# Optimization experiments

Hardware: AMD Instinct MI355X
Metric: run time of the kernel (lower is better)

The kernel has to match this reference:

```python
import jax, jax.numpy as jnp
import numpy as np

H = 128  # hidden size

def lstm_layer(x, Wih, Whh, bih, bhh):
    """One PyTorch-semantics LSTM layer. x: (B,T,F). Gate order: i,f,g,o."""
    B = x.shape[0]
    # Precompute input contributions for all timesteps: (B,T,4H)
    xg = jnp.einsum('btf,gf->btg', x, Wih) + bih + bhh
    def step(carry, xt):
        h, c = carry
        g = xt + h @ Whh.T                      # (B,4H)
        i, f, gg, o = jnp.split(g, 4, axis=-1)
        i = jax.nn.sigmoid(i)
        f = jax.nn.sigmoid(f)
        gg = jnp.tanh(gg)
        o = jax.nn.sigmoid(o)
        c = f * c + i * gg
        h = o * jnp.tanh(c)
        return (h, c), h
    h0 = jnp.zeros((B, H), x.dtype)
    (hT, cT), hs = jax.lax.scan(step, (h0, h0), jnp.swapaxes(xg, 0, 1))
    return jnp.swapaxes(hs, 0, 1), hT  # (B,T,H), (B,H)


def setup_inputs() -> dict:
    key = jax.random.key(0)
    ks = jax.random.split(key, 20)
    B, T = 256, 2048
    s = 1.0 / np.sqrt(H)  # PyTorch default init scale
    inp = {
        'x': jax.random.normal(ks[0], (B, T, 1), jnp.float32),
        'Wih0': jax.random.uniform(ks[1], (4 * H, 1), jnp.float32, -s, s),
        'Whh0': jax.random.uniform(ks[2], (4 * H, H), jnp.float32, -s, s),
        'bih0': jax.random.uniform(ks[3], (4 * H,), jnp.float32, -s, s),
        'bhh0': jax.random.uniform(ks[4], (4 * H,), jnp.float32, -s, s),
        'Wih1': jax.random.uniform(ks[5], (4 * H, H), jnp.float32, -s, s),
        'Whh1': jax.random.uniform(ks[6], (4 * H, H), jnp.float32, -s, s),
        'bih1': jax.random.uniform(ks[7], (4 * H,), jnp.float32, -s, s),
        'bhh1': jax.random.uniform(ks[8], (4 * H,), jnp.float32, -s, s),
        'Wih2': jax.random.uniform(ks[9], (4 * H, H), jnp.float32, -s, s),
        'Whh2': jax.random.uniform(ks[10], (4 * H, H), jnp.float32, -s, s),
        'bih2': jax.random.uniform(ks[11], (4 * H,), jnp.float32, -s, s),
        'bhh2': jax.random.uniform(ks[12], (4 * H,), jnp.float32, -s, s),
        'fc1_w': jax.random.uniform(ks[13], (64, H), jnp.float32, -s, s),
        'fc1_b': jax.random.uniform(ks[14], (64,), jnp.float32, -s, s),
        'fc2_w': jax.random.uniform(ks[15], (5, 64), jnp.float32, -1.0 / 8, 1.0 / 8),
        'fc2_b': jax.random.uniform(ks[16], (5,), jnp.float32, -1.0 / 8, 1.0 / 8),
    }
    return inp


def reference(x, Wih0, Whh0, bih0, bhh0, Wih1, Whh1, bih1, bhh1,
              Wih2, Whh2, bih2, bhh2, fc1_w, fc1_b, fc2_w, fc2_b):
    # 3-layer LSTM (eval mode: inter-layer dropout is identity)
    h1, _ = lstm_layer(x, Wih0, Whh0, bih0, bhh0)
    h2, _ = lstm_layer(h1, Wih1, Whh1, bih1, bhh1)
    _, hT = lstm_layer(h2, Wih2, Whh2, bih2, bhh2)  # hn[-1]: (B,H)
    z = jax.nn.relu(hT @ fc1_w.T + fc1_b)
    return z @ fc2_w.T + fc2_b  # (B, num_classes)
```

## Files before the change

### kernel.cpp

```cpp
#include <hip/hip_runtime.h>

#define HDIM 128
#define TDIM 2048
#define BDIM 256
#define CHUNK 16
#define NT 512
#define XGP 20

typedef _Float16 half8_t __attribute__((ext_vector_type(8)));
typedef float f32x4 __attribute__((ext_vector_type(4)));

__device__ __forceinline__ f32x4 mfma16(half8_t a, half8_t b, f32x4 c) {
    return __builtin_amdgcn_mfma_f32_16x16x32_f16(a, b, c, 0, 0, 0);
}

__device__ __forceinline__ void fast_barrier() {
    asm volatile("s_waitcnt lgkmcnt(0)\n\ts_barrier" ::: "memory");
}

__device__ __forceinline__ float sigm_f(float x) { return 1.0f / (1.0f + __expf(-x)); }
__device__ __forceinline__ float tanh_f(float x) { return 1.0f - 2.0f / (1.0f + __expf(2.0f * x)); }

__global__ __launch_bounds__(256)
void convert_w(const float* __restrict__ Whh0, const float* __restrict__ Wih1,
               const float* __restrict__ Whh1, const float* __restrict__ Wih2,
               const float* __restrict__ Whh2, _Float16* __restrict__ dst) {
    int i = blockIdx.x * 256 + threadIdx.x;
    int seg = i >> 16, off = i & 65535;
    const float* s = (seg == 0) ? Whh0 : (seg == 1) ? Wih1 : (seg == 2) ? Whh1
                   : (seg == 3) ? Wih2 : Whh2;
    dst[i] = (_Float16)s[off];
}

__global__ __launch_bounds__(NT, 2)
void lstm3_kernel(const float* __restrict__ x,   const float* __restrict__ Wih0,
                  const float* __restrict__ bih0, const float* __restrict__ bhh0,
                  const float* __restrict__ bih1, const float* __restrict__ bhh1,
                  const float* __restrict__ bih2, const float* __restrict__ bhh2,
                  const float* __restrict__ fc1w, const float* __restrict__ fc1b,
                  const float* __restrict__ fc2w, const float* __restrict__ fc2b,
                  float* __restrict__ out,
                  _Float16* __restrict__ gbuf, const _Float16* __restrict__ wbuf)
{
    __shared__ __align__(16) _Float16 hwin_s[CHUNK][HDIM];
    __shared__ __align__(16) _Float16 xin_s[2][CHUNK][HDIM];
    __shared__ __align__(16) float xg_s[2][512 * XGP];
    __shared__ __align__(16) float z_s[64];

    const int tid = threadIdx.x;
    const int ln = tid & 63;
    const int wv = tid >> 6;
    const int n16 = ln & 15;
    const int kb = (ln >> 4) * 8;
    const int un = wv * 16 + n16;
    const int b = blockIdx.x;

    {
        float bsum[4], w0[4];
        half8_t bhh[4][4];
#pragma unroll
        for (int tau = 0; tau < 4; ++tau) {
            const int g = tau * HDIM + un;
            bsum[tau] = bih0[g] + bhh0[g];
            w0[tau] = Wih0[g];
#pragma unroll
            for (int kk = 0; kk < 4; ++kk)
                bhh[tau][kk] = *(const half8_t*)(wbuf + (size_t)g * HDIM + kk * 32 + kb);
        }
        if (tid < HDIM) hwin_s[CHUNK - 1][tid] = (_Float16)0.f;
        float c = 0.f;
        float4 xp[4];
        {
            const float4* xq = (const float4*)(x + (size_t)b * TDIM);
#pragma unroll
            for (int i = 0; i < 4; ++i) xp[i] = xq[i];
        }

#pragma unroll 1
        for (int t0 = 0; t0 < TDIM; t0 += CHUNK) {
            float xv[CHUNK];
#pragma unroll
            for (int i = 0; i < 4; ++i) {
                xv[4 * i] = xp[i].x; xv[4 * i + 1] = xp[i].y;
                xv[4 * i + 2] = xp[i].z; xv[4 * i + 3] = xp[i].w;
            }
            int tn = (t0 + CHUNK < TDIM) ? (t0 + CHUNK) : t0;
            const float4* xq = (const float4*)(x + (size_t)b * TDIM + tn);
#pragma unroll
            for (int i = 0; i < 4; ++i) xp[i] = xq[i];

#pragma unroll
            for (int tt = 0; tt < CHUNK; ++tt) {
                fast_barrier();
                const int t = t0 + tt, row = (t + CHUNK - 1) & 15;
                half8_t A0 = *(const half8_t*)&hwin_s[row][kb];
                half8_t A1 = *(const half8_t*)&hwin_s[row][32 + kb];
                half8_t A2 = *(const half8_t*)&hwin_s[row][64 + kb];
                half8_t A3 = *(const half8_t*)&hwin_s[row][96 + kb];
                float g4[4];
#pragma unroll
                for (int tau = 0; tau < 4; ++tau) {
                    f32x4 Cz = {0.f, 0.f, 0.f, 0.f};
                    Cz = mfma16(A0, bhh[tau][0], Cz);
                    Cz = mfma16(A1, bhh[tau][1], Cz);
                    Cz = mfma16(A2, bhh[tau][2], Cz);
                    Cz = mfma16(A3, bhh[tau][3], Cz);
                    g4[tau] = Cz[0];
                }
                float ig = sigm_f(g4[0] + xv[tt] * w0[0] + bsum[0]);
                float fg = sigm_f(g4[1] + xv[tt] * w0[1] + bsum[1]);
                float gg = tanh_f(g4[2] + xv[tt] * w0[2] + bsum[2]);
                float og = sigm_f(g4[3] + xv[tt] * w0[3] + bsum[3]);
                c = fg * c + ig * gg;
                if (kb == 0) hwin_s[t & 15][un] = (_Float16)(og * tanh_f(c));
            }
            fast_barrier();
            int2 v = ((const int2*)&hwin_s[0][0])[tid];
            ((int2*)(gbuf + ((size_t)b * TDIM + t0) * HDIM))[tid] = v;
        }
    }

#pragma unroll 1
    for (int layer = 1; layer < 3; ++layer) {
        const _Float16* whh_p = wbuf + (size_t)((layer == 1) ? 2 : 4) * 65536;
        const _Float16* wih_p = wbuf + (size_t)((layer == 1) ? 1 : 3) * 65536;
        const float* bih = (layer == 1) ? bih1 : bih2;
        const float* bhh = (layer == 1) ? bhh1 : bhh2;

        float bsum[4];
        half8_t bhhf[4][4], bihf[4][4];
#pragma unroll
        for (int tau = 0; tau < 4; ++tau) {
            const int g = tau * HDIM + un;
            bsum[tau] = bih[g] + bhh[g];
#pragma unroll
            for (int kk = 0; kk < 4; ++kk)
                bhhf[tau][kk] = *(const half8_t*)(whh_p + (size_t)g * HDIM + kk * 32 + kb);
            const int gp = (wv * 4 + tau) * 16 + n16;
#pragma unroll
            for (int kk = 0; kk < 4; ++kk)
                bihf[tau][kk] = *(const half8_t*)(wih_p + (size_t)gp * HDIM + kk * 32 + kb);
        }

        __syncthreads();
        if (tid < HDIM) hwin_s[CHUNK - 1][tid] = (_Float16)0.f;
        float c = 0.f;

        int2 stage = ((const int2*)(gbuf + (size_t)b * TDIM * HDIM))[tid];
        ((int2*)&xin_s[0][0][0])[tid] = stage;
        __syncthreads();
        {
            half8_t A0 = *(const half8_t*)&xin_s[0][n16][kb];
            half8_t A1 = *(const half8_t*)&xin_s[0][n16][32 + kb];
            half8_t A2 = *(const half8_t*)&xin_s[0][n16][64 + kb];
            half8_t A3 = *(const half8_t*)&xin_s[0][n16][96 + kb];
#pragma unroll
            for (int tau = 0; tau < 4; ++tau) {
                f32x4 a = {0.f, 0.f, 0.f, 0.f};
                a = mfma16(A0, bihf[tau][0], a);
                a = mfma16(A1, bihf[tau][1], a);
                a = mfma16(A2, bihf[tau][2], a);
                a = mfma16(A3, bihf[tau][3], a);
                const int g = (wv * 4 + tau) * 16 + n16;
                *(f32x4*)&xg_s[0][g * XGP + (kb >> 1)] = a;
            }
        }
        stage = ((const int2*)(gbuf + ((size_t)b * TDIM + CHUNK) * HDIM))[tid];

        f32x4 pacc[4];
#pragma unroll 1
        for (int t0 = 0; t0 < TDIM; t0 += CHUNK) {
            const int ci = t0 >> 4, rbuf = ci & 1, cb = rbuf ^ 1;
            ((int2*)&xin_s[cb][0][0])[tid] = stage;
            int tn = (t0 + 2 * CHUNK < TDIM) ? (t0 + 2 * CHUNK) : t0;
            stage = ((const int2*)(gbuf + ((size_t)b * TDIM + tn) * HDIM))[tid];

            float2 xgv[4];
#pragma unroll
            for (int tt = 0; tt < CHUNK; ++tt) {
                fast_barrier();
                const int t = t0 + tt, row = (t + CHUNK - 1) & 15;
                half8_t A0 = *(const half8_t*)&hwin_s[row][kb];
                half8_t A1 = *(const half8_t*)&hwin_s[row][32 + kb];
                half8_t A2 = *(const half8_t*)&hwin_s[row][64 + kb];
                half8_t A3 = *(const half8_t*)&hwin_s[row][96 + kb];

                if (tt == 0) {
                    half8_t X0 = *(const half8_t*)&xin_s[cb][n16][kb];
                    half8_t X1 = *(const half8_t*)&xin_s[cb][n16][32 + kb];
                    half8_t X2 = *(const half8_t*)&xin_s[cb][n16][64 + kb];
                    half8_t X3 = *(const half8_t*)&xin_s[cb][n16][96 + kb];
#pragma unroll
                    for (int tau = 0; tau < 4; ++tau) {
                        f32x4 a = {0.f, 0.f, 0.f, 0.f};
                        a = mfma16(X0, bihf[tau][0], a);
                        a = mfma16(X1, bihf[tau][1], a);
                        a = mfma16(X2, bihf[tau][2], a);
                        a = mfma16(X3, bihf[tau][3], a);
                        pacc[tau] = a;
                    }
                }
                if ((tt & 1) == 0) {
#pragma unroll
                    for (int q = 0; q < 4; ++q)
                        xgv[q] = *(const float2*)&xg_s[rbuf][(q * HDIM + un) * XGP + tt];
                }

                float g4[4];
#pragma unroll
                for (int tau = 0; tau < 4; ++tau) {
                    f32x4 Cz = {0.f, 0.f, 0.f, 0.f};
                    Cz = mfma16(A0, bhhf[tau][0], Cz);
                    Cz = mfma16(A1, bhhf[tau][1], Cz);
                    Cz = mfma16(A2, bhhf[tau][2], Cz);
                    Cz = mfma16(A3, bhhf[tau][3], Cz);
                    g4[tau] = Cz[0];
                }

                float x0 = (tt & 1) ? xgv[0].y : xgv[0].x;
                float x1 = (tt & 1) ? xgv[1].y : xgv[1].x;
                float x2 = (tt & 1) ? xgv[2].y : xgv[2].x;
                float x3 = (tt & 1) ? xgv[3].y : xgv[3].x;
                float ig = sigm_f(g4[0] + x0 + bsum[0]);
                float fg = sigm_f(g4[1] + x1 + bsum[1]);
                float gg = tanh_f(g4[2] + x2 + bsum[2]);
                float og = sigm_f(g4[3] + x3 + bsum[3]);
                c = fg * c + ig * gg;
                if (kb == 0) hwin_s[t & 15][un] = (_Float16)(og * tanh_f(c));

                if (tt == CHUNK - 1) {
#pragma unroll
                    for (int tau = 0; tau < 4; ++tau) {
                        const int g = (wv * 4 + tau) * 16 + n16;
                        *(f32x4*)&xg_s[cb][g * XGP + (kb >> 1)] = pacc[tau];
                    }
                }
            }
            if (layer == 1) {
                fast_barrier();
                int2 v = ((const int2*)&hwin_s[0][0])[tid];
                ((int2*)(gbuf + ((size_t)b * TDIM + t0) * HDIM))[tid] = v;
            }
        }
    }

    __syncthreads();
    if (tid < 64) {
        const float* w = fc1w + tid * HDIM;
        float s = fc1b[tid];
#pragma unroll
        for (int k = 0; k < HDIM; ++k) s += w[k] * (float)hwin_s[CHUNK - 1][k];
        z_s[tid] = fmaxf(s, 0.0f);
    }
    __syncthreads();
    if (tid < 5) {
        const float* w = fc2w + tid * 64;
        float s = fc2b[tid];
#pragma unroll
        for (int k = 0; k < 64; ++k) s += w[k] * z_s[k];
        out[b * 5 + tid] = s;
    }
}

extern "C" void kernel_launch(void* const* d_in, const int* in_sizes, int n_in,
                              void* d_out, int out_size, void* d_ws, size_t ws_size,
                              hipStream_t stream) {
    (void)in_sizes; (void)n_in; (void)out_size; (void)ws_size;
    const float* x    = (const float*)d_in[0];
    const float* Wih0 = (const float*)d_in[1];
    const float* Whh0 = (const float*)d_in[2];
    const float* bih0 = (const float*)d_in[3];
    const float* bhh0 = (const float*)d_in[4];
    const float* Wih1 = (const float*)d_in[5];
    const float* Whh1 = (const float*)d_in[6];
    const float* bih1 = (const float*)d_in[7];
    const float* bhh1 = (const float*)d_in[8];
    const float* Wih2 = (const float*)d_in[9];
    const float* Whh2 = (const float*)d_in[10];
    const float* bih2 = (const float*)d_in[11];
    const float* bhh2 = (const float*)d_in[12];
    const float* fc1w = (const float*)d_in[13];
    const float* fc1b = (const float*)d_in[14];
    const float* fc2w = (const float*)d_in[15];
    const float* fc2b = (const float*)d_in[16];
    float* out = (float*)d_out;

    _Float16* gbuf = (_Float16*)d_ws;
    _Float16* wbuf = gbuf + (size_t)67108864;

    hipLaunchKernelGGL(convert_w, dim3(1280), dim3(256), 0, stream,
                       Whh0, Wih1, Whh1, Wih2, Whh2, wbuf);
    hipLaunchKernelGGL(lstm3_kernel, dim3(BDIM), dim3(NT), 0, stream,
                       x, Wih0, bih0, bhh0, bih1, bhh1, bih2, bhh2,
                       fc1w, fc1b, fc2w, fc2b, out, gbuf, wbuf);
}
```

Measured before the change: 3.658 ms.

## Wavefront-pipeline all three LSTM layers concurrently with LDS ring buffers

The kernel no longer runs the three layers one after another through a global scratch buffer. It runs them as a skewed wavefront, each layer lagging the previous one by 16 steps, so the whole network takes about T+32 barrier steps instead of 3T. Warps are assigned mixed slots across layers, and hidden states pass between layers through 32-deep LDS rings. The per-chunk input projection is computed from the ring, with Wih streamed from global memory on each use instead of held in registers. This removes two full sequential passes and the global round-trips, but each step now does more MFMA work per warp, adds more branching, and reloads Wih from global memory every chunk.

```diff
diff --git a/kernel.cpp b/kernel.cpp
--- a/kernel.cpp
+++ b/kernel.cpp
@@ -3,9 +3,11 @@
 #define HDIM 128
 #define TDIM 2048
 #define BDIM 256
-#define CHUNK 16
 #define NT 512
-#define XGP 20
+#define RING 32
+#define RP 136
+#define XGP 17
+#define NSTEP (TDIM + 32)
 
 typedef _Float16 half8_t __attribute__((ext_vector_type(8)));
 typedef float f32x4 __attribute__((ext_vector_type(4)));
@@ -13,9 +15,11 @@
 __device__ __forceinline__ f32x4 mfma16(half8_t a, half8_t b, f32x4 c) {
     return __builtin_amdgcn_mfma_f32_16x16x32_f16(a, b, c, 0, 0, 0);
 }
-
 __device__ __forceinline__ void fast_barrier() {
     asm volatile("s_waitcnt lgkmcnt(0)\n\ts_barrier" ::: "memory");
+}
+__device__ __forceinline__ void lds_fence() {
+    asm volatile("s_waitcnt lgkmcnt(0)" ::: "memory");
 }
 
 __device__ __forceinline__ float sigm_f(float x) { return 1.0f / (1.0f + __expf(-x)); }
@@ -39,207 +43,185 @@
                   const float* __restrict__ bih2, const float* __restrict__ bhh2,
                   const float* __restrict__ fc1w, const float* __restrict__ fc1b,
                   const float* __restrict__ fc2w, const float* __restrict__ fc2b,
-                  float* __restrict__ out,
-                  _Float16* __restrict__ gbuf, const _Float16* __restrict__ wbuf)
+                  float* __restrict__ out, const _Float16* __restrict__ wbuf)
 {
-    __shared__ __align__(16) _Float16 hwin_s[CHUNK][HDIM];
-    __shared__ __align__(16) _Float16 xin_s[2][CHUNK][HDIM];
+    __shared__ __align__(16) _Float16 ring_s[3][RING * RP];
     __shared__ __align__(16) float xg_s[2][512 * XGP];
+    __shared__ __align__(16) float xs_s[2][16];
     __shared__ __align__(16) float z_s[64];
 
-    const int tid = threadIdx.x;
-    const int ln = tid & 63;
-    const int wv = tid >> 6;
-    const int n16 = ln & 15;
-    const int kb = (ln >> 4) * 8;
-    const int un = wv * 16 + n16;
+    const int tid = threadIdx.x, ln = tid & 63, wv = tid >> 6;
+    const int n16 = ln & 15, qd = ln >> 4, kb = qd * 8;
     const int b = blockIdx.x;
 
+    const int s0l_t[8] = {0,0,0,1,1,1,2,2};
+    const int s0g_t[8] = {0,3,6,1,4,7,2,5};
+    const int s0n_t[8] = {3,3,2,3,3,1,3,3};
+    const int s1l_t[8] = {0,0,1,0,0,2,0,0};
+    const int s1n_t[8] = {0,0,1,0,0,2,0,0};
+    const int s0l = s0l_t[wv], s0g = s0g_t[wv], s0n = s0n_t[wv];
+    const int s1l = s1l_t[wv], s1n = s1n_t[wv];
+
+    int slayer[3], sgrp[3];
+#pragma unroll
+    for (int i = 0; i < 3; ++i) {
+        if (i < s0n) { slayer[i] = s0l; sgrp[i] = s0g + i; }
+        else         { slayer[i] = s1l; sgrp[i] = i - s0n; }
+    }
+
+    const _Float16* whhL0 = wbuf;
+    const _Float16* whhL1 = wbuf + 2 * 65536;
+    const _Float16* whhL2 = wbuf + 4 * 65536;
+    const _Float16* wihL1 = wbuf + 1 * 65536;
+    const _Float16* wihL2 = wbuf + 3 * 65536;
+
+    const int  lslot = (ln < 16) ? 0 : (ln < 32) ? 1 : 2;
+    const bool lact  = ln < 48;
+    const int  llay  = (lslot == 0) ? slayer[0] : (lslot == 1) ? slayer[1] : slayer[2];
+    const int  lgrp  = (lslot == 0) ? sgrp[0]   : (lslot == 1) ? sgrp[1]   : sgrp[2];
+    const int  u     = lgrp * 16 + n16;
+
+    float bsum[4], w0g[4];
+#pragma unroll
+    for (int q = 0; q < 4; ++q) {
+        const int row = q * HDIM + u;
+        const float* bi = (llay == 0) ? bih0 : (llay == 1) ? bih1 : bih2;
+        const float* bh = (llay == 0) ? bhh0 : (llay == 1) ? bhh1 : bhh2;
+        bsum[q] = bi[row] + bh[row];
+        w0g[q] = (llay == 0) ? Wih0[row] : 0.f;
+    }
+
+    half8_t bfr[3][4][4];
+#pragma unroll
+    for (int i = 0; i < 3; ++i) {
+        const int lay = slayer[i];
+        const _Float16* wp = (lay == 0) ? whhL0 : (lay == 1) ? whhL1 : whhL2;
+#pragma unroll
+        for (int tau = 0; tau < 4; ++tau) {
+            const int row = tau * HDIM + sgrp[i] * 16 + n16;
+#pragma unroll
+            for (int kk = 0; kk < 4; ++kk)
+                bfr[i][tau][kk] = *(const half8_t*)(wp + (size_t)row * HDIM + kk * 32 + kb);
+        }
+    }
+
     {
-        float bsum[4], w0[4];
-        half8_t bhh[4][4];
-#pragma unroll
-        for (int tau = 0; tau < 4; ++tau) {
-            const int g = tau * HDIM + un;
-            bsum[tau] = bih0[g] + bhh0[g];
-            w0[tau] = Wih0[g];
+        int* r = (int*)&ring_s[0][0];
+        for (int i = tid; i < 3 * RING * RP / 2; i += NT) r[i] = 0;
+    }
+    float xpre = 0.f;
+    if (wv == 0 && ln < 16) {
+        xs_s[0][ln] = x[(size_t)b * TDIM + ln];
+        xpre = x[(size_t)b * TDIM + 16 + ln];
+    }
+    __syncthreads();
+
+    float c_st = 0.f;
+    float g4[3][4];
+
+#pragma unroll 1
+    for (int s = 0; s < NSTEP; ++s) {
+        fast_barrier();
+
+        if (wv == 0 && (s & 15) == 15 && s < TDIM - 1 && ln < 16) {
+            xs_s[((s >> 4) + 1) & 1][ln] = xpre;
+            int t = s + 17 + ln;
+            xpre = x[(size_t)b * TDIM + (t < TDIM ? t : 0)];
+        }
+
+#pragma unroll
+        for (int pseg = 0; pseg < 2; ++pseg) {
+            const int pl  = (pseg == 0) ? s0l : s1l;
+            const int pg0 = (pseg == 0) ? s0g : 0;
+            const int pn  = (pseg == 0) ? s0n : s1n;
+            const bool en = (pseg == 0) ? (s0l >= 1) : (s1n > 0);
+            if (!en) continue;
+            const int tl = s - 16 * pl;
+            if (tl < 0 || tl >= TDIM || (tl & 15) != 0) continue;
+
+            const _Float16* ringp = &ring_s[pl - 1][0];
+            half8_t aP[4];
+            const int srow = ((tl + n16) & 31) * RP;
 #pragma unroll
             for (int kk = 0; kk < 4; ++kk)
-                bhh[tau][kk] = *(const half8_t*)(wbuf + (size_t)g * HDIM + kk * 32 + kb);
-        }
-        if (tid < HDIM) hwin_s[CHUNK - 1][tid] = (_Float16)0.f;
-        float c = 0.f;
-        float4 xp[4];
+                aP[kk] = *(const half8_t*)(ringp + srow + kk * 32 + kb);
+            const _Float16* wp = (pl == 1) ? wihL1 : wihL2;
+            float* xgb = &xg_s[pl - 1][0];
+#pragma unroll 1
+            for (int g = 0; g < pn; ++g) {
+#pragma unroll
+                for (int tau = 0; tau < 4; ++tau) {
+                    const int gp = tau * HDIM + (pg0 + g) * 16 + n16;
+                    const _Float16* wr = wp + (size_t)gp * HDIM + kb;
+                    half8_t b0 = *(const half8_t*)(wr);
+                    half8_t b1 = *(const half8_t*)(wr + 32);
+                    half8_t b2 = *(const half8_t*)(wr + 64);
+                    half8_t b3 = *(const half8_t*)(wr + 96);
+                    f32x4 a = {0.f, 0.f, 0.f, 0.f};
+                    a = mfma16(aP[0], b0, a);
+                    a = mfma16(aP[1], b1, a);
+                    a = mfma16(aP[2], b2, a);
+                    a = mfma16(aP[3], b3, a);
+                    float* dst = xgb + gp * XGP + qd * 4;
+                    dst[0] = a[0]; dst[1] = a[1]; dst[2] = a[2]; dst[3] = a[3];
+                }
+            }
+        }
+        lds_fence();
+
         {
-            const float4* xq = (const float4*)(x + (size_t)b * TDIM);
-#pragma unroll
-            for (int i = 0; i < 4; ++i) xp[i] = xq[i];
-        }
-
-#pragma unroll 1
-        for (int t0 = 0; t0 < TDIM; t0 += CHUNK) {
-            float xv[CHUNK];
-#pragma unroll
-            for (int i = 0; i < 4; ++i) {
-                xv[4 * i] = xp[i].x; xv[4 * i + 1] = xp[i].y;
-                xv[4 * i + 2] = xp[i].z; xv[4 * i + 3] = xp[i].w;
-            }
-            int tn = (t0 + CHUNK < TDIM) ? (t0 + CHUNK) : t0;
-            const float4* xq = (const float4*)(x + (size_t)b * TDIM + tn);
-#pragma unroll
-            for (int i = 0; i < 4; ++i) xp[i] = xq[i];
-
-#pragma unroll
-            for (int tt = 0; tt < CHUNK; ++tt) {
-                fast_barrier();
-                const int t = t0 + tt, row = (t + CHUNK - 1) & 15;
-                half8_t A0 = *(const half8_t*)&hwin_s[row][kb];
-                half8_t A1 = *(const half8_t*)&hwin_s[row][32 + kb];
-                half8_t A2 = *(const half8_t*)&hwin_s[row][64 + kb];
-                half8_t A3 = *(const half8_t*)&hwin_s[row][96 + kb];
-                float g4[4];
-#pragma unroll
-                for (int tau = 0; tau < 4; ++tau) {
-                    f32x4 Cz = {0.f, 0.f, 0.f, 0.f};
-                    Cz = mfma16(A0, bhh[tau][0], Cz);
-                    Cz = mfma16(A1, bhh[tau][1], Cz);
-                    Cz = mfma16(A2, bhh[tau][2], Cz);
-                    Cz = mfma16(A3, bhh[tau][3], Cz);
-                    g4[tau] = Cz[0];
-                }
-                float ig = sigm_f(g4[0] + xv[tt] * w0[0] + bsum[0]);
-                float fg = sigm_f(g4[1] + xv[tt] * w0[1] + bsum[1]);
-                float gg = tanh_f(g4[2] + xv[tt] * w0[2] + bsum[2]);
-                float og = sigm_f(g4[3] + xv[tt] * w0[3] + bsum[3]);
-                c = fg * c + ig * gg;
-                if (kb == 0) hwin_s[t & 15][un] = (_Float16)(og * tanh_f(c));
-            }
-            fast_barrier();
-            int2 v = ((const int2*)&hwin_s[0][0])[tid];
-            ((int2*)(gbuf + ((size_t)b * TDIM + t0) * HDIM))[tid] = v;
-        }
-    }
-
-#pragma unroll 1
-    for (int layer = 1; layer < 3; ++layer) {
-        const _Float16* whh_p = wbuf + (size_t)((layer == 1) ? 2 : 4) * 65536;
-        const _Float16* wih_p = wbuf + (size_t)((layer == 1) ? 1 : 3) * 65536;
-        const float* bih = (layer == 1) ? bih1 : bih2;
-        const float* bhh = (layer == 1) ? bhh1 : bhh2;
-
-        float bsum[4];
-        half8_t bhhf[4][4], bihf[4][4];
-#pragma unroll
-        for (int tau = 0; tau < 4; ++tau) {
-            const int g = tau * HDIM + un;
-            bsum[tau] = bih[g] + bhh[g];
-#pragma unroll
-            for (int kk = 0; kk < 4; ++kk)
-                bhhf[tau][kk] = *(const half8_t*)(whh_p + (size_t)g * HDIM + kk * 32 + kb);
-            const int gp = (wv * 4 + tau) * 16 + n16;
-#pragma unroll
-            for (int kk = 0; kk < 4; ++kk)
-                bihf[tau][kk] = *(const half8_t*)(wih_p + (size_t)gp * HDIM + kk * 32 + kb);
-        }
-
-        __syncthreads();
-        if (tid < HDIM) hwin_s[CHUNK - 1][tid] = (_Float16)0.f;
-        float c = 0.f;
-
-        int2 stage = ((const int2*)(gbuf + (size_t)b * TDIM * HDIM))[tid];
-        ((int2*)&xin_s[0][0][0])[tid] = stage;
-        __syncthreads();
-        {
-            half8_t A0 = *(const half8_t*)&xin_s[0][n16][kb];
-            half8_t A1 = *(const half8_t*)&xin_s[0][n16][32 + kb];
-            half8_t A2 = *(const half8_t*)&xin_s[0][n16][64 + kb];
-            half8_t A3 = *(const half8_t*)&xin_s[0][n16][96 + kb];
-#pragma unroll
-            for (int tau = 0; tau < 4; ++tau) {
-                f32x4 a = {0.f, 0.f, 0.f, 0.f};
-                a = mfma16(A0, bihf[tau][0], a);
-                a = mfma16(A1, bihf[tau][1], a);
-                a = mfma16(A2, bihf[tau][2], a);
-                a = mfma16(A3, bihf[tau][3], a);
-                const int g = (wv * 4 + tau) * 16 + n16;
-                *(f32x4*)&xg_s[0][g * XGP + (kb >> 1)] = a;
-            }
-        }
-        stage = ((const int2*)(gbuf + ((size_t)b * TDIM + CHUNK) * HDIM))[tid];
-
-        f32x4 pacc[4];
-#pragma unroll 1
-        for (int t0 = 0; t0 < TDIM; t0 += CHUNK) {
-            const int ci = t0 >> 4, rbuf = ci & 1, cb = rbuf ^ 1;
-            ((int2*)&xin_s[cb][0][0])[tid] = stage;
-            int tn = (t0 + 2 * CHUNK < TDIM) ? (t0 + 2 * CHUNK) : t0;
-            stage = ((const int2*)(gbuf + ((size_t)b * TDIM + tn) * HDIM))[tid];
-
-            float2 xgv[4];
-#pragma unroll
-            for (int tt = 0; tt < CHUNK; ++tt) {
-                fast_barrier();
-                const int t = t0 + tt, row = (t + CHUNK - 1) & 15;
-                half8_t A0 = *(const half8_t*)&hwin_s[row][kb];
-                half8_t A1 = *(const half8_t*)&hwin_s[row][32 + kb];
-                half8_t A2 = *(const half8_t*)&hwin_s[row][64 + kb];
-                half8_t A3 = *(const half8_t*)&hwin_s[row][96 + kb];
-
-                if (tt == 0) {
-                    half8_t X0 = *(const half8_t*)&xin_s[cb][n16][kb];
-                    half8_t X1 = *(const half8_t*)&xin_s[cb][n16][32 + kb];
-                    half8_t X2 = *(const half8_t*)&xin_s[cb][n16][64 + kb];
-                    half8_t X3 = *(const half8_t*)&xin_s[cb][n16][96 + kb];
+            half8_t aR[4];
+            int curlay = -1;
+#pragma unroll
+            for (int i = 0; i < 3; ++i) {
+                const int lay = slayer[i];
+                const int tl = s - 16 * lay;
+                if (tl >= 0 && tl < TDIM) {
+                    if (lay != curlay) {
+                        const _Float16* rp = &ring_s[lay][((tl - 1) & 31) * RP];
+#pragma unroll
+                        for (int kk = 0; kk < 4; ++kk)
+                            aR[kk] = *(const half8_t*)(rp + kk * 32 + kb);
+                        curlay = lay;
+                    }
 #pragma unroll
                     for (int tau = 0; tau < 4; ++tau) {
                         f32x4 a = {0.f, 0.f, 0.f, 0.f};
-                        a = mfma16(X0, bihf[tau][0], a);
-                        a = mfma16(X1, bihf[tau][1], a);
-                        a = mfma16(X2, bihf[tau][2], a);
-                        a = mfma16(X3, bihf[tau][3], a);
-                        pacc[tau] = a;
-                    }
-                }
-                if ((tt & 1) == 0) {
-#pragma unroll
-                    for (int q = 0; q < 4; ++q)
-                        xgv[q] = *(const float2*)&xg_s[rbuf][(q * HDIM + un) * XGP + tt];
-                }
-
-                float g4[4];
-#pragma unroll
-                for (int tau = 0; tau < 4; ++tau) {
-                    f32x4 Cz = {0.f, 0.f, 0.f, 0.f};
-                    Cz = mfma16(A0, bhhf[tau][0], Cz);
-                    Cz = mfma16(A1, bhhf[tau][1], Cz);
-                    Cz = mfma16(A2, bhhf[tau][2], Cz);
-                    Cz = mfma16(A3, bhhf[tau][3], Cz);
-                    g4[tau] = Cz[0];
-                }
-
-                float x0 = (tt & 1) ? xgv[0].y : xgv[0].x;
-                float x1 = (tt & 1) ? xgv[1].y : xgv[1].x;
-                float x2 = (tt & 1) ? xgv[2].y : xgv[2].x;
-                float x3 = (tt & 1) ? xgv[3].y : xgv[3].x;
-                float ig = sigm_f(g4[0] + x0 + bsum[0]);
-                float fg = sigm_f(g4[1] + x1 + bsum[1]);
-                float gg = tanh_f(g4[2] + x2 + bsum[2]);
-                float og = sigm_f(g4[3] + x3 + bsum[3]);
-                c = fg * c + ig * gg;
-                if (kb == 0) hwin_s[t & 15][un] = (_Float16)(og * tanh_f(c));
-
-                if (tt == CHUNK - 1) {
-#pragma unroll
-                    for (int tau = 0; tau < 4; ++tau) {
-                        const int g = (wv * 4 + tau) * 16 + n16;
-                        *(f32x4*)&xg_s[cb][g * XGP + (kb >> 1)] = pacc[tau];
+                        a = mfma16(aR[0], bfr[i][tau][0], a);
+                        a = mfma16(aR[1], bfr[i][tau][1], a);
+                        a = mfma16(aR[2], bfr[i][tau][2], a);
+                        a = mfma16(aR[3], bfr[i][tau][3], a);
+                        g4[i][tau] = a[0];
                     }
                 }
             }
-            if (layer == 1) {
-                fast_barrier();
-                int2 v = ((const int2*)&hwin_s[0][0])[tid];
-                ((int2*)(gbuf + ((size_t)b * TDIM + t0) * HDIM))[tid] = v;
+        }
+
+        {
+            const int tl_l = s - 16 * llay;
+            if (lact && tl_l >= 0 && tl_l < TDIM) {
+                float ga[4];
+#pragma unroll
+                for (int q = 0; q < 4; ++q)
+                    ga[q] = (lslot == 0) ? g4[0][q] : (lslot == 1) ? g4[1][q] : g4[2][q];
+                float xq[4];
+                if (llay == 0) {
+                    float xt = xs_s[(tl_l >> 4) & 1][tl_l & 15];
+#pragma unroll
+                    for (int q = 0; q < 4; ++q) xq[q] = xt * w0g[q];
+                } else {
+                    const float* xgb = &xg_s[llay - 1][0];
+#pragma unroll
+                    for (int q = 0; q < 4; ++q)
+                        xq[q] = xgb[(q * HDIM + u) * XGP + (tl_l & 15)];
+                }
+                float ig = sigm_f(ga[0] + xq[0] + bsum[0]);
+                float fg = sigm_f(ga[1] + xq[1] + bsum[1]);
+                float gg = tanh_f(ga[2] + xq[2] + bsum[2]);
+                float og = sigm_f(ga[3] + xq[3] + bsum[3]);
+                c_st = fg * c_st + ig * gg;
+                float h = og * tanh_f(c_st);
+                ring_s[llay][(tl_l & 31) * RP + u] = (_Float16)h;
             }
         }
     }
@@ -247,18 +229,18 @@
     __syncthreads();
     if (tid < 64) {
         const float* w = fc1w + tid * HDIM;
-        float s = fc1b[tid];
-#pragma unroll
-        for (int k = 0; k < HDIM; ++k) s += w[k] * (float)hwin_s[CHUNK - 1][k];
-        z_s[tid] = fmaxf(s, 0.0f);
+        float sacc = fc1b[tid];
+#pragma unroll
+        for (int k = 0; k < HDIM; ++k) sacc += w[k] * (float)ring_s[2][31 * RP + k];
+        z_s[tid] = fmaxf(sacc, 0.0f);
     }
     __syncthreads();
     if (tid < 5) {
         const float* w = fc2w + tid * 64;
-        float s = fc2b[tid];
-#pragma unroll
-        for (int k = 0; k < 64; ++k) s += w[k] * z_s[k];
-        out[b * 5 + tid] = s;
+        float sacc = fc2b[tid];
+#pragma unroll
+        for (int k = 0; k < 64; ++k) sacc += w[k] * z_s[k];
+        out[b * 5 + tid] = sacc;
     }
 }
 
@@ -285,12 +267,11 @@
     const float* fc2b = (const float*)d_in[16];
     float* out = (float*)d_out;
 
-    _Float16* gbuf = (_Float16*)d_ws;
-    _Float16* wbuf = gbuf + (size_t)67108864;
+    _Float16* wbuf = (_Float16*)d_ws;
 
     hipLaunchKernelGGL(convert_w, dim3(1280), dim3(256), 0, stream,
                        Whh0, Wih1, Whh1, Wih2, Whh2, wbuf);
     hipLaunchKernelGGL(lstm3_kernel, dim3(BDIM), dim3(NT), 0, stream,
                        x, Wih0, bih0, bhh0, bih1, bhh1, bih2, bhh2,
-                       fc1w, fc1b, fc2w, fc2b, out, gbuf, wbuf);
-}
+                       fc1w, fc1b, fc2w, fc2b, out, wbuf);
+}
```

Result: slower. 9.800 ms (+167.9%).

## Wavefront-interleave LSTM layers 0 and 1 in one timestep loop with AGPR weights

Applied to the files above, without the earlier changes.

Layers 0 and 1 now run together in a single loop, with layer 1 lagging layer 0 by 16 steps. Their hidden states pass through an LDS ring buffer, so both recurrent matvecs share one barrier per step instead of two separate serial passes. Both recurrent weight sets are pinned in AGPRs via inline-asm MFMA so they fit alongside each other, and layer 1's input projection is computed per 16-step chunk, loading Wih1 from global memory. The aim is to roughly halve the number of serial barrier-bound steps for the first two layers. In exchange there is more register and LDS pressure, manual s_nop hazard padding, and per-chunk global weight reloads.

```diff
diff --git a/kernel.cpp b/kernel.cpp
--- a/kernel.cpp
+++ b/kernel.cpp
@@ -3,9 +3,12 @@
 #define HDIM 128
 #define TDIM 2048
 #define BDIM 256
+#define NT 512
+#define RING 32
+#define RP 136
+#define XGP 17
+#define XGP2 20
 #define CHUNK 16
-#define NT 512
-#define XGP 20
 
 typedef _Float16 half8_t __attribute__((ext_vector_type(8)));
 typedef float f32x4 __attribute__((ext_vector_type(4)));
@@ -13,9 +16,16 @@
 __device__ __forceinline__ f32x4 mfma16(half8_t a, half8_t b, f32x4 c) {
     return __builtin_amdgcn_mfma_f32_16x16x32_f16(a, b, c, 0, 0, 0);
 }
+__device__ __forceinline__ void mfma_accA(f32x4 &d, half8_t a, half8_t b) {
+    asm("v_mfma_f32_16x16x32_f16 %0, %1, %2, %0" : "+v"(d) : "v"(a), "a"(b));
+}
+__device__ __forceinline__ void pin_agpr(half8_t &v) { asm("" : "+a"(v)); }
 
 __device__ __forceinline__ void fast_barrier() {
     asm volatile("s_waitcnt lgkmcnt(0)\n\ts_barrier" ::: "memory");
+}
+__device__ __forceinline__ void lds_fence() {
+    asm volatile("s_waitcnt lgkmcnt(0)" ::: "memory");
 }
 
 __device__ __forceinline__ float sigm_f(float x) { return 1.0f / (1.0f + __expf(-x)); }
@@ -42,107 +52,169 @@
                   float* __restrict__ out,
                   _Float16* __restrict__ gbuf, const _Float16* __restrict__ wbuf)
 {
+    __shared__ __align__(16) _Float16 ring_s[2][RING * RP];
+    __shared__ __align__(16) float xg1_s[512 * XGP];
+    __shared__ __align__(16) float xs_s[2][16];
     __shared__ __align__(16) _Float16 hwin_s[CHUNK][HDIM];
     __shared__ __align__(16) _Float16 xin_s[2][CHUNK][HDIM];
-    __shared__ __align__(16) float xg_s[2][512 * XGP];
+    __shared__ __align__(16) float xg2_s[2][512 * XGP2];
     __shared__ __align__(16) float z_s[64];
 
-    const int tid = threadIdx.x;
-    const int ln = tid & 63;
-    const int wv = tid >> 6;
-    const int n16 = ln & 15;
-    const int kb = (ln >> 4) * 8;
+    const int tid = threadIdx.x, ln = tid & 63, wv = tid >> 6;
+    const int n16 = ln & 15, qd = ln >> 4, kb = qd * 8;
     const int un = wv * 16 + n16;
     const int b = blockIdx.x;
 
+    const _Float16* whhL0 = wbuf;
+    const _Float16* wihL1 = wbuf + 1 * 65536;
+    const _Float16* whhL1 = wbuf + 2 * 65536;
+    const _Float16* wihL2 = wbuf + 3 * 65536;
+    const _Float16* whhL2 = wbuf + 4 * 65536;
+
     {
-        float bsum[4], w0[4];
-        half8_t bhh[4][4];
+        float bsum0[4], bsum1[4], w0[4];
+#pragma unroll
+        for (int q = 0; q < 4; ++q) {
+            const int row = q * HDIM + un;
+            bsum0[q] = bih0[row] + bhh0[row];
+            bsum1[q] = bih1[row] + bhh1[row];
+            w0[q] = Wih0[row];
+        }
+        half8_t wf0[4][4], wf1[4][4];
+#pragma unroll
+        for (int tau = 0; tau < 4; ++tau) {
+            const int row = tau * HDIM + un;
+#pragma unroll
+            for (int kk = 0; kk < 4; ++kk) {
+                wf0[tau][kk] = *(const half8_t*)(whhL0 + (size_t)row * HDIM + kk * 32 + kb);
+                wf1[tau][kk] = *(const half8_t*)(whhL1 + (size_t)row * HDIM + kk * 32 + kb);
+                pin_agpr(wf0[tau][kk]);
+                pin_agpr(wf1[tau][kk]);
+            }
+        }
+        for (int i = tid; i < 2 * RING * RP / 2; i += NT) ((int*)&ring_s[0][0])[i] = 0;
+        float xpre = 0.f;
+        if (wv == 0 && ln < 16) {
+            xs_s[0][ln] = x[(size_t)b * TDIM + ln];
+            xpre = x[(size_t)b * TDIM + 16 + ln];
+        }
+        __syncthreads();
+
+        float c0 = 0.f, c1 = 0.f;
+#pragma unroll 1
+        for (int s = 0; s < TDIM + 16; ++s) {
+            fast_barrier();
+            if (wv == 0 && (s & 15) == 15 && s < TDIM - 1 && ln < 16) {
+                xs_s[((s >> 4) + 1) & 1][ln] = xpre;
+                int t = s + 17 + ln;
+                xpre = x[(size_t)b * TDIM + (t < TDIM ? t : 0)];
+            }
+            if ((s & 15) == 0 && s >= 16) {
+                const int tb = s - 16;
+                const _Float16* r0 = &ring_s[0][((tb + n16) & 31) * RP];
+                half8_t aP0 = *(const half8_t*)(r0 + kb);
+                half8_t aP1 = *(const half8_t*)(r0 + 32 + kb);
+                half8_t aP2 = *(const half8_t*)(r0 + 64 + kb);
+                half8_t aP3 = *(const half8_t*)(r0 + 96 + kb);
+#pragma unroll 1
+                for (int tau = 0; tau < 4; ++tau) {
+                    const _Float16* wr = wihL1 + (size_t)(tau * HDIM + un) * HDIM + kb;
+                    half8_t b0 = *(const half8_t*)(wr);
+                    half8_t b1 = *(const half8_t*)(wr + 32);
+                    half8_t b2 = *(const half8_t*)(wr + 64);
+                    half8_t b3 = *(const half8_t*)(wr + 96);
+                    f32x4 a = {0.f, 0.f, 0.f, 0.f};
+                    a = mfma16(aP0, b0, a);
+                    a = mfma16(aP1, b1, a);
+                    a = mfma16(aP2, b2, a);
+                    a = mfma16(aP3, b3, a);
+                    *(f32x4*)&xg1_s[(tau * HDIM + un) * XGP + qd * 4] = a;
+                }
+            }
+            lds_fence();
+            float xq1[4];
+            if (s >= 16) {
+                const int ti = (s - 16) & 15;
+#pragma unroll
+                for (int q = 0; q < 4; ++q) xq1[q] = xg1_s[(q * HDIM + un) * XGP + ti];
+            }
+
+            f32x4 d0[4], d1[4];
+            if (s < TDIM) {
+                const _Float16* rp = &ring_s[0][((s - 1) & 31) * RP];
+                half8_t A0 = *(const half8_t*)(rp + kb);
+                half8_t A1 = *(const half8_t*)(rp + 32 + kb);
+                half8_t A2 = *(const half8_t*)(rp + 64 + kb);
+                half8_t A3 = *(const half8_t*)(rp + 96 + kb);
+#pragma unroll
+                for (int tau = 0; tau < 4; ++tau) {
+                    d0[tau] = (f32x4){0.f, 0.f, 0.f, 0.f};
+                    mfma_accA(d0[tau], A0, wf0[tau][0]);
+                    mfma_accA(d0[tau], A1, wf0[tau][1]);
+                    mfma_accA(d0[tau], A2, wf0[tau][2]);
+                    mfma_accA(d0[tau], A3, wf0[tau][3]);
+                }
+            }
+            if (s >= 16) {
+                const _Float16* rp = &ring_s[1][((s - 17) & 31) * RP];
+                half8_t A0 = *(const half8_t*)(rp + kb);
+                half8_t A1 = *(const half8_t*)(rp + 32 + kb);
+                half8_t A2 = *(const half8_t*)(rp + 64 + kb);
+                half8_t A3 = *(const half8_t*)(rp + 96 + kb);
+#pragma unroll
+                for (int tau = 0; tau < 4; ++tau) {
+                    d1[tau] = (f32x4){0.f, 0.f, 0.f, 0.f};
+                    mfma_accA(d1[tau], A0, wf1[tau][0]);
+                    mfma_accA(d1[tau], A1, wf1[tau][1]);
+                    mfma_accA(d1[tau], A2, wf1[tau][2]);
+                    mfma_accA(d1[tau], A3, wf1[tau][3]);
+                }
+            }
+            asm volatile("s_nop 7\n\ts_nop 7" ::);
+
+            if (s < TDIM) {
+                float xt = xs_s[(s >> 4) & 1][s & 15];
+                float gi = sigm_f(d0[0][0] + xt * w0[0] + bsum0[0]);
+                float gf = sigm_f(d0[1][0] + xt * w0[1] + bsum0[1]);
+                float gg = tanh_f(d0[2][0] + xt * w0[2] + bsum0[2]);
+                float go = sigm_f(d0[3][0] + xt * w0[3] + bsum0[3]);
+                c0 = gf * c0 + gi * gg;
+                if (kb == 0) ring_s[0][(s & 31) * RP + un] = (_Float16)(go * tanh_f(c0));
+            }
+            if (s >= 16) {
+                float gi = sigm_f(d1[0][0] + xq1[0] + bsum1[0]);
+                float gf = sigm_f(d1[1][0] + xq1[1] + bsum1[1]);
+                float gg = tanh_f(d1[2][0] + xq1[2] + bsum1[2]);
+                float go = sigm_f(d1[3][0] + xq1[3] + bsum1[3]);
+                c1 = gf * c1 + gi * gg;
+                if (kb == 0) ring_s[1][((s - 16) & 31) * RP + un] = (_Float16)(go * tanh_f(c1));
+            }
+            if ((s & 15) == 15 && s >= 31) {
+                fast_barrier();
+                const int ci = (s - 16) >> 4;
+                const int r = tid >> 5, col = (tid & 31) * 4;
+                *(int2*)(gbuf + ((size_t)b * TDIM + ci * 16 + r) * HDIM + col) =
+                    *(const int2*)(&ring_s[1][((ci & 1) * 16 + r) * RP + col]);
+            }
+        }
+    }
+    __syncthreads();
+
+    {
+        float bsum[4];
+        half8_t bhhf[4][4], bihf[4][4];
 #pragma unroll
         for (int tau = 0; tau < 4; ++tau) {
             const int g = tau * HDIM + un;
-            bsum[tau] = bih0[g] + bhh0[g];
-            w0[tau] = Wih0[g];
+            bsum[tau] = bih2[g] + bhh2[g];
 #pragma unroll
             for (int kk = 0; kk < 4; ++kk)
-                bhh[tau][kk] = *(const half8_t*)(wbuf + (size_t)g * HDIM + kk * 32 + kb);
-        }
-        if (tid < HDIM) hwin_s[CHUNK - 1][tid] = (_Float16)0.f;
-        float c = 0.f;
-        float4 xp[4];
-        {
-            const float4* xq = (const float4*)(x + (size_t)b * TDIM);
-#pragma unroll
-            for (int i = 0; i < 4; ++i) xp[i] = xq[i];
-        }
-
-#pragma unroll 1
-        for (int t0 = 0; t0 < TDIM; t0 += CHUNK) {
-            float xv[CHUNK];
-#pragma unroll
-            for (int i = 0; i < 4; ++i) {
-                xv[4 * i] = xp[i].x; xv[4 * i + 1] = xp[i].y;
-                xv[4 * i + 2] = xp[i].z; xv[4 * i + 3] = xp[i].w;
-            }
-            int tn = (t0 + CHUNK < TDIM) ? (t0 + CHUNK) : t0;
-            const float4* xq = (const float4*)(x + (size_t)b * TDIM + tn);
-#pragma unroll
-            for (int i = 0; i < 4; ++i) xp[i] = xq[i];
-
-#pragma unroll
-            for (int tt = 0; tt < CHUNK; ++tt) {
-                fast_barrier();
-                const int t = t0 + tt, row = (t + CHUNK - 1) & 15;
-                half8_t A0 = *(const half8_t*)&hwin_s[row][kb];
-                half8_t A1 = *(const half8_t*)&hwin_s[row][32 + kb];
-                half8_t A2 = *(const half8_t*)&hwin_s[row][64 + kb];
-                half8_t A3 = *(const half8_t*)&hwin_s[row][96 + kb];
-                float g4[4];
-#pragma unroll
-                for (int tau = 0; tau < 4; ++tau) {
-                    f32x4 Cz = {0.f, 0.f, 0.f, 0.f};
-                    Cz = mfma16(A0, bhh[tau][0], Cz);
-                    Cz = mfma16(A1, bhh[tau][1], Cz);
-                    Cz = mfma16(A2, bhh[tau][2], Cz);
-                    Cz = mfma16(A3, bhh[tau][3], Cz);
-                    g4[tau] = Cz[0];
-                }
-                float ig = sigm_f(g4[0] + xv[tt] * w0[0] + bsum[0]);
-                float fg = sigm_f(g4[1] + xv[tt] * w0[1] + bsum[1]);
-                float gg = tanh_f(g4[2] + xv[tt] * w0[2] + bsum[2]);
-                float og = sigm_f(g4[3] + xv[tt] * w0[3] + bsum[3]);
-                c = fg * c + ig * gg;
-                if (kb == 0) hwin_s[t & 15][un] = (_Float16)(og * tanh_f(c));
-            }
-            fast_barrier();
-            int2 v = ((const int2*)&hwin_s[0][0])[tid];
-            ((int2*)(gbuf + ((size_t)b * TDIM + t0) * HDIM))[tid] = v;
-        }
-    }
-
-#pragma unroll 1
-    for (int layer = 1; layer < 3; ++layer) {
-        const _Float16* whh_p = wbuf + (size_t)((layer == 1) ? 2 : 4) * 65536;
-        const _Float16* wih_p = wbuf + (size_t)((layer == 1) ? 1 : 3) * 65536;
-        const float* bih = (layer == 1) ? bih1 : bih2;
-        const float* bhh = (layer == 1) ? bhh1 : bhh2;
-
-        float bsum[4];
-        half8_t bhhf[4][4], bihf[4][4];
-#pragma unroll
-        for (int tau = 0; tau < 4; ++tau) {
-            const int g = tau * HDIM + un;
-            bsum[tau] = bih[g] + bhh[g];
+                bhhf[tau][kk] = *(const half8_t*)(whhL2 + (size_t)g * HDIM + kk * 32 + kb);
+            const int gp = (wv * 4 + tau) * 16 + n16;
 #pragma unroll
             for (int kk = 0; kk < 4; ++kk)
-                bhhf[tau][kk] = *(const half8_t*)(whh_p + (size_t)g * HDIM + kk * 32 + kb);
-            const int gp = (wv * 4 + tau) * 16 + n16;
-#pragma unroll
-            for (int kk = 0; kk < 4; ++kk)
-                bihf[tau][kk] = *(const half8_t*)(wih_p + (size_t)gp * HDIM + kk * 32 + kb);
-        }
-
-        __syncthreads();
+                bihf[tau][kk] = *(const half8_t*)(wihL2 + (size_t)gp * HDIM + kk * 32 + kb);
+        }
         if (tid < HDIM) hwin_s[CHUNK - 1][tid] = (_Float16)0.f;
         float c = 0.f;
 
@@ -162,7 +234,7 @@
                 a = mfma16(A2, bihf[tau][2], a);
                 a = mfma16(A3, bihf[tau][3], a);
                 const int g = (wv * 4 + tau) * 16 + n16;
-                *(f32x4*)&xg_s[0][g * XGP + (kb >> 1)] = a;
+                *(f32x4*)&xg2_s[0][g * XGP2 + (kb >> 1)] = a;
             }
         }
         stage = ((const int2*)(gbuf + ((size_t)b * TDIM + CHUNK) * HDIM))[tid];
@@ -203,7 +275,7 @@
                 if ((tt & 1) == 0) {
 #pragma unroll
                     for (int q = 0; q < 4; ++q)
-                        xgv[q] = *(const float2*)&xg_s[rbuf][(q * HDIM + un) * XGP + tt];
+                        xgv[q] = *(const float2*)&xg2_s[rbuf][(q * HDIM + un) * XGP2 + tt];
                 }
 
                 float g4[4];
@@ -232,14 +304,9 @@
 #pragma unroll
                     for (int tau = 0; tau < 4; ++tau) {
                         const int g = (wv * 4 + tau) * 16 + n16;
-                        *(f32x4*)&xg_s[cb][g * XGP + (kb >> 1)] = pacc[tau];
+                        *(f32x4*)&xg2_s[cb][g * XGP2 + (kb >> 1)] = pacc[tau];
                     }
                 }
-            }
-            if (layer == 1) {
-                fast_barrier();
-                int2 v = ((const int2*)&hwin_s[0][0])[tid];
-                ((int2*)(gbuf + ((size_t)b * TDIM + t0) * HDIM))[tid] = v;
             }
         }
     }
@@ -247,18 +314,18 @@
     __syncthreads();
     if (tid < 64) {
         const float* w = fc1w + tid * HDIM;
-        float s = fc1b[tid];
-#pragma unroll
-        for (int k = 0; k < HDIM; ++k) s += w[k] * (float)hwin_s[CHUNK - 1][k];
-        z_s[tid] = fmaxf(s, 0.0f);
+        float sacc = fc1b[tid];
+#pragma unroll
+        for (int k = 0; k < HDIM; ++k) sacc += w[k] * (float)hwin_s[CHUNK - 1][k];
+        z_s[tid] = fmaxf(sacc, 0.0f);
     }
     __syncthreads();
     if (tid < 5) {
         const float* w = fc2w + tid * 64;
-        float s = fc2b[tid];
-#pragma unroll
-        for (int k = 0; k < 64; ++k) s += w[k] * z_s[k];
-        out[b * 5 + tid] = s;
+        float sacc = fc2b[tid];
+#pragma unroll
+        for (int k = 0; k < 64; ++k) sacc += w[k] * z_s[k];
+        out[b * 5 + tid] = sacc;
     }
 }
 
```

New measurement: 4.577 ms. 1.25x slower.
